# Performance work log

Measured on AMD Instinct MI355X. Metric: run time of the kernel, lower is better.

Reference implementation:

```python
import jax, jax.numpy as jnp
import numpy as np
from jax import lax

DIM = 512
HEADS = 8
SR = 2  # kernel_and_stride for the KV downsampling conv


def setup_inputs() -> dict:
    key = jax.random.key(0)
    k0, k1, k2, k3 = jax.random.split(key, 4)
    B, C, H, W = 4, DIM, 64, 64
    x = jax.random.normal(k0, (B, C, H, W), dtype=jnp.float32)
    # Conv weights in OIHW layout (matching torch)
    wq = jax.random.normal(k1, (C, C, 1, 1), dtype=jnp.float32) / np.sqrt(C)
    wkv = jax.random.normal(k2, (2 * C, C, SR, SR), dtype=jnp.float32) / np.sqrt(C * SR * SR)
    wout = jax.random.normal(k3, (C, C, 1, 1), dtype=jnp.float32) / np.sqrt(C)
    return {"x": x, "wq": wq, "wkv": wkv, "wout": wout}


def _attend(x, wq, wkv, wout):
    B, C, H, W = x.shape
    d = C // HEADS
    scale = d ** -0.5
    # to_q: 1x1 conv == channel matmul
    q = jnp.einsum('bchw,oc->bohw', x, wq[:, :, 0, 0])
    # to_kv: strided conv, downsamples spatial grid by SR
    kv = lax.conv_general_dilated(
        x, wkv, window_strides=(SR, SR), padding='VALID',
        dimension_numbers=('NCHW', 'OIHW', 'NCHW'))
    k, v = jnp.split(kv, 2, axis=1)  # each [B, C, H/SR, W/SR]

    def to_bhl(t):  # [B, (h d), X, Y] -> [B, h, X*Y, d]
        b, c, xh, xw = t.shape
        return t.reshape(b, HEADS, d, xh * xw).transpose(0, 1, 3, 2)

    qh, kh, vh = to_bhl(q), to_bhl(k), to_bhl(v)
    sim = jnp.einsum('bhid,bhjd->bhij', qh, kh) * scale
    attn = jax.nn.softmax(sim, axis=-1)
    out = jnp.einsum('bhij,bhjd->bhid', attn, vh)  # [B, h, HW, d]
    out = out.transpose(0, 1, 3, 2).reshape(B, C, H, W)
    return jnp.einsum('bchw,oc->bohw', out, wout[:, :, 0, 0])


def reference(x, wq, wkv, wout):
    return _attend(x, wq, wkv, wout)
```

## Files before the change

kernel.cpp:

```cpp
#include <hip/hip_runtime.h>
#include <hip/hip_bf16.h>

typedef __bf16 bf16x8 __attribute__((ext_vector_type(8)));
typedef float f32x4 __attribute__((ext_vector_type(4)));
typedef unsigned short ushort_t;
typedef ushort_t ushort8 __attribute__((ext_vector_type(8)));
typedef unsigned uint2v __attribute__((ext_vector_type(2)));
typedef unsigned uint4v __attribute__((ext_vector_type(4)));

#define DIM 512
#define HEADS 8
#define HD 64
#define HWN 4096
#define KVN 1024
#define KKV 2048
#define LOG2E 1.44269504f

__device__ __forceinline__ ushort_t f2bf(float f) {
    union { float f; unsigned u; } v; v.f = f;
    unsigned r = v.u + 0x7fffu + ((v.u >> 16) & 1u);
    return (ushort_t)(r >> 16);
}

__device__ __forceinline__ unsigned cvtpk(float lo, float hi) {
    unsigned r;
    asm("v_cvt_pk_bf16_f32 %0, %1, %2" : "=v"(r) : "v"(lo), "v"(hi));
    return r;
}

__device__ __forceinline__ void pl32swap(unsigned &a, unsigned &b) {
    asm("v_permlane32_swap_b32 %0, %1" : "+v"(a), "+v"(b));
}
__device__ __forceinline__ void pl16swap(unsigned &a, unsigned &b) {
    asm("v_permlane16_swap_b32 %0, %1" : "+v"(a), "+v"(b));
}

__device__ __forceinline__ bf16x8 frag4(unsigned a, unsigned b, unsigned c, unsigned d) {
    uint4v t; t[0] = a; t[1] = b; t[2] = c; t[3] = d;
    return __builtin_bit_cast(bf16x8, t);
}

__device__ __forceinline__ void gload_lds16(const ushort_t* g, ushort_t* l) {
    __builtin_amdgcn_global_load_lds(
        (const __attribute__((address_space(1))) unsigned int*)(const void*)g,
        (__attribute__((address_space(3))) unsigned int*)(void*)l,
        16, 0, 0);
}

__global__ __launch_bounds__(256) void cvt_kernel(
        const float* __restrict__ src, ushort_t* __restrict__ dst, int n8) {
    int i = blockIdx.x * 256 + threadIdx.x;
    if (i >= n8) return;
    const float* p = &src[(size_t)i * 8];
    f32x4 v0 = *(const f32x4*)&p[0];
    f32x4 v1 = *(const f32x4*)&p[4];
    ushort8 w;
    w[0] = f2bf(v0[0]); w[1] = f2bf(v0[1]); w[2] = f2bf(v0[2]); w[3] = f2bf(v0[3]);
    w[4] = f2bf(v1[0]); w[5] = f2bf(v1[1]); w[6] = f2bf(v1[2]); w[7] = f2bf(v1[3]);
    *(ushort8*)&dst[i * 8] = w;
}

__global__ __launch_bounds__(256) void cvt_xT_kernel(
        const float* __restrict__ x, ushort_t* __restrict__ xT) {
    const int b  = blockIdx.z;
    const int c0 = blockIdx.y * 64;
    const int p0 = blockIdx.x * 64;
    __shared__ ushort_t tile[64 * 72];

    const int tid = threadIdx.x;
    {
        int r = tid >> 2, pc = (tid & 3) * 16;
        const float* src = &x[((size_t)b * DIM + c0 + r) * HWN + p0 + pc];
        f32x4 v0 = *(const f32x4*)&src[0];
        f32x4 v1 = *(const f32x4*)&src[4];
        f32x4 v2 = *(const f32x4*)&src[8];
        f32x4 v3 = *(const f32x4*)&src[12];
        ushort8 w0, w1;
        w0[0]=f2bf(v0[0]); w0[1]=f2bf(v0[1]); w0[2]=f2bf(v0[2]); w0[3]=f2bf(v0[3]);
        w0[4]=f2bf(v1[0]); w0[5]=f2bf(v1[1]); w0[6]=f2bf(v1[2]); w0[7]=f2bf(v1[3]);
        w1[0]=f2bf(v2[0]); w1[1]=f2bf(v2[1]); w1[2]=f2bf(v2[2]); w1[3]=f2bf(v2[3]);
        w1[4]=f2bf(v3[0]); w1[5]=f2bf(v3[1]); w1[6]=f2bf(v3[2]); w1[7]=f2bf(v3[3]);
        *(ushort8*)&tile[r * 72 + pc]     = w0;
        *(ushort8*)&tile[r * 72 + pc + 8] = w1;
    }
    __syncthreads();
    {
        int p = tid >> 2, cc = (tid & 3) * 16;
        ushort8 w0, w1;
        #pragma unroll
        for (int j = 0; j < 8; ++j) {
            w0[j] = tile[(cc + j) * 72 + p];
            w1[j] = tile[(cc + 8 + j) * 72 + p];
        }
        ushort_t* dst = &xT[((size_t)b * HWN + p0 + p) * DIM + c0 + cc];
        *(ushort8*)&dst[0] = w0;
        *(ushort8*)&dst[8] = w1;
    }
}

__global__ __launch_bounds__(256) void cvt_wkvT_kernel(
        const float* __restrict__ wkv, ushort_t* __restrict__ wkvT) {
    int i = blockIdx.x * 256 + threadIdx.x;
    if (i >= 1024 * 512) return;
    int o2 = i >> 9, c = i & 511;
    f32x4 v = *(const f32x4*)&wkv[(size_t)i * 4];
    #pragma unroll
    for (int q = 0; q < 4; ++q)
        wkvT[(size_t)o2 * KKV + q * 512 + c] = f2bf(v[q]);
}

__global__ __launch_bounds__(256) void qproj_kernel(
        const ushort_t* __restrict__ xT, const ushort_t* __restrict__ wqb,
        ushort_t* __restrict__ qs) {
    const int b  = blockIdx.z;
    const int m0 = blockIdx.y * 64;
    const int p0 = blockIdx.x * 64;

    __shared__ ushort_t ldsA[64 * 40];
    __shared__ ushort_t ldsB[64 * 40];

    const int tid  = threadIdx.x;
    const int wave = tid >> 6;
    const int lane = tid & 63;
    const int l15  = lane & 15;
    const int quad = lane >> 4;
    const int mw   = (wave >> 1) * 32;
    const int nw   = (wave & 1) * 32;

    f32x4 zero = {0.f, 0.f, 0.f, 0.f};
    f32x4 acc[2][2] = {{zero, zero}, {zero, zero}};

    for (int k0 = 0; k0 < DIM; k0 += 32) {
        int row = tid >> 2, ko = (tid & 3) * 8;
        *(ushort8*)&ldsA[row * 40 + ko] =
            *(const ushort8*)&wqb[(m0 + row) * DIM + k0 + ko];
        *(ushort8*)&ldsB[row * 40 + ko] =
            *(const ushort8*)&xT[((size_t)b * HWN + p0 + row) * DIM + k0 + ko];
        __syncthreads();
        bf16x8 a0 = *(const bf16x8*)&ldsA[(mw + l15) * 40 + quad * 8];
        bf16x8 a1 = *(const bf16x8*)&ldsA[(mw + 16 + l15) * 40 + quad * 8];
        bf16x8 b0 = *(const bf16x8*)&ldsB[(nw + l15) * 40 + quad * 8];
        bf16x8 b1 = *(const bf16x8*)&ldsB[(nw + 16 + l15) * 40 + quad * 8];
        acc[0][0] = __builtin_amdgcn_mfma_f32_16x16x32_bf16(a0, b0, acc[0][0], 0, 0, 0);
        acc[0][1] = __builtin_amdgcn_mfma_f32_16x16x32_bf16(a0, b1, acc[0][1], 0, 0, 0);
        acc[1][0] = __builtin_amdgcn_mfma_f32_16x16x32_bf16(a1, b0, acc[1][0], 0, 0, 0);
        acc[1][1] = __builtin_amdgcn_mfma_f32_16x16x32_bf16(a1, b1, acc[1][1], 0, 0, 0);
        __syncthreads();
    }

    #pragma unroll
    for (int mi = 0; mi < 2; ++mi)
        #pragma unroll
        for (int ni = 0; ni < 2; ++ni)
            #pragma unroll
            for (int r = 0; r < 4; ++r) {
                int m = m0 + mw + mi * 16 + quad * 4 + r;
                int n = p0 + nw + ni * 16 + l15;
                qs[((size_t)b * DIM + m) * HWN + n] =
                    f2bf(acc[mi][ni][r] * (0.125f * LOG2E));
            }
}

__global__ __launch_bounds__(256) void kv_kernel(
        const ushort_t* __restrict__ xT, const ushort_t* __restrict__ wkvT,
        ushort_t* __restrict__ ks, ushort_t* __restrict__ vt) {
    const int b  = blockIdx.z;
    const int m0 = blockIdx.y * 64;
    const int j0 = blockIdx.x * 64;

    __shared__ ushort_t ldsA[64 * 40];
    __shared__ ushort_t ldsB[64 * 40];
    __shared__ ushort_t cbuf[64 * 72];

    const int tid  = threadIdx.x;
    const int wave = tid >> 6;
    const int lane = tid & 63;
    const int l15  = lane & 15;
    const int quad = lane >> 4;
    const int mw   = (wave >> 1) * 32;
    const int nw   = (wave & 1) * 32;

    f32x4 zero = {0.f, 0.f, 0.f, 0.f};
    f32x4 acc[2][2] = {{zero, zero}, {zero, zero}};

    const int row = tid >> 2, ko = (tid & 3) * 8;
    const int yj = (j0 + row) >> 5, xj = (j0 + row) & 31;

    for (int k0 = 0; k0 < KKV; k0 += 32) {
        int q  = k0 >> 9;
        int c0 = k0 & 511;
        int di = q >> 1, dj = q & 1;
        int p  = (2 * yj + di) * 64 + 2 * xj + dj;
        *(ushort8*)&ldsA[row * 40 + ko] =
            *(const ushort8*)&wkvT[(size_t)(m0 + row) * KKV + k0 + ko];
        *(ushort8*)&ldsB[row * 40 + ko] =
            *(const ushort8*)&xT[((size_t)b * HWN + p) * DIM + c0 + ko];
        __syncthreads();
        bf16x8 a0 = *(const bf16x8*)&ldsA[(mw + l15) * 40 + quad * 8];
        bf16x8 a1 = *(const bf16x8*)&ldsA[(mw + 16 + l15) * 40 + quad * 8];
        bf16x8 b0 = *(const bf16x8*)&ldsB[(nw + l15) * 40 + quad * 8];
        bf16x8 b1 = *(const bf16x8*)&ldsB[(nw + 16 + l15) * 40 + quad * 8];
        acc[0][0] = __builtin_amdgcn_mfma_f32_16x16x32_bf16(a0, b0, acc[0][0], 0, 0, 0);
        acc[0][1] = __builtin_amdgcn_mfma_f32_16x16x32_bf16(a0, b1, acc[0][1], 0, 0, 0);
        acc[1][0] = __builtin_amdgcn_mfma_f32_16x16x32_bf16(a1, b0, acc[1][0], 0, 0, 0);
        acc[1][1] = __builtin_amdgcn_mfma_f32_16x16x32_bf16(a1, b1, acc[1][1], 0, 0, 0);
        __syncthreads();
    }

    if (m0 < DIM) {
        int h = m0 >> 6;
        #pragma unroll
        for (int mi = 0; mi < 2; ++mi)
            #pragma unroll
            for (int ni = 0; ni < 2; ++ni)
                #pragma unroll
                for (int r = 0; r < 4; ++r) {
                    int m = mw + mi * 16 + quad * 4 + r;
                    int n = nw + ni * 16 + l15;
                    cbuf[n * 72 + m] = f2bf(acc[mi][ni][r]);
                }
        __syncthreads();
        int n = tid >> 2, mo = (tid & 3) * 16;
        ushort8 v0 = *(const ushort8*)&cbuf[n * 72 + mo];
        ushort8 v1 = *(const ushort8*)&cbuf[n * 72 + mo + 8];
        ushort_t* dst = &ks[(((size_t)b * HEADS + h) * KVN + j0 + n) * HD + mo];
        *(ushort8*)&dst[0] = v0;
        *(ushort8*)&dst[8] = v1;
    } else {
        int h = (m0 - DIM) >> 6;
        #pragma unroll
        for (int mi = 0; mi < 2; ++mi)
            #pragma unroll
            for (int ni = 0; ni < 2; ++ni)
                #pragma unroll
                for (int r = 0; r < 4; ++r) {
                    int dd = mw + mi * 16 + quad * 4 + r;
                    int n  = nw + ni * 16 + l15;
                    vt[(((size_t)b * HEADS + h) * HD + dd) * KVN + j0 + n] =
                        f2bf(acc[mi][ni][r]);
                }
    }
}

__global__ __launch_bounds__(256, 2) void attn_kernel(
        const ushort_t* __restrict__ qs,
        const ushort_t* __restrict__ ks,
        const ushort_t* __restrict__ vt,
        ushort_t* __restrict__ ao) {
    const int b = blockIdx.z, h = blockIdx.y;
    const int tid = threadIdx.x, wave = tid >> 6, lane = tid & 63;
    const int l15 = lane & 15, quad = lane >> 4;
    const int s7  = l15 & 7;
    const int iw = blockIdx.x * 256 + wave * 64;

    __shared__ ushort_t ldsK[2][64 * 64];
    __shared__ ushort_t ldsV[2][64 * 64];

    const ushort_t* Kh = &ks[((size_t)b * HEADS + h) * (KVN * HD)];
    const ushort_t* Vh = &vt[((size_t)b * HEADS + h) * (HD * KVN)];

    const int srow = wave * 8 + (lane >> 3);
    const int schk = (lane & 7) ^ (lane >> 3);
    const ushort_t* kp0 = Kh + srow * HD + schk * 8;
    const ushort_t* kp1 = Kh + (srow + 32) * HD + schk * 8;
    const ushort_t* vp0 = Vh + (size_t)srow * KVN + schk * 8;
    const ushort_t* vp1 = Vh + (size_t)(srow + 32) * KVN + schk * 8;

    bf16x8 bq[4][2];
    #pragma unroll
    for (int ih = 0; ih < 4; ++ih)
        #pragma unroll
        for (int kk = 0; kk < 2; ++kk) {
            ushort8 t;
            #pragma unroll
            for (int j = 0; j < 8; ++j) {
                int c = h * HD + kk * 32 + quad * 8 + j;
                int p = iw + ih * 16 + l15;
                t[j] = qs[((size_t)b * DIM + c) * HWN + p];
            }
            bq[ih][kk] = *(bf16x8*)&t;
        }

    f32x4 zero = {0.f, 0.f, 0.f, 0.f};
    f32x4 o[4][4];
    #pragma unroll
    for (int ih = 0; ih < 4; ++ih)
        #pragma unroll
        for (int nt = 0; nt < 4; ++nt) o[ih][nt] = zero;
    float ssum[4] = {0.f, 0.f, 0.f, 0.f};

    gload_lds16(kp0, &ldsK[0][wave * 512]);
    gload_lds16(kp1, &ldsK[0][wave * 512 + 2048]);
    gload_lds16(vp0, &ldsV[0][wave * 512]);
    gload_lds16(vp1, &ldsV[0][wave * 512 + 2048]);
    asm volatile("s_waitcnt vmcnt(0)" ::: "memory");
    __syncthreads();

    for (int t = 0; t < 16; ++t) {
        const int cur = t & 1;
        if (t < 15) {
            const int jn = (t + 1) * 64;
            gload_lds16(kp0 + jn * HD, &ldsK[cur ^ 1][wave * 512]);
            gload_lds16(kp1 + jn * HD, &ldsK[cur ^ 1][wave * 512 + 2048]);
            gload_lds16(vp0 + jn,      &ldsV[cur ^ 1][wave * 512]);
            gload_lds16(vp1 + jn,      &ldsV[cur ^ 1][wave * 512 + 2048]);
        }

        unsigned P2[4][4][2];
        #pragma unroll
        for (int nt = 0; nt < 4; ++nt) {
            const ushort_t* kb = &ldsK[cur][(nt * 16 + l15) * 64];
            bf16x8 bk0 = *(const bf16x8*)&kb[(quad ^ s7) * 8];
            bf16x8 bk1 = *(const bf16x8*)&kb[((quad + 4) ^ s7) * 8];
            #pragma unroll
            for (int ih = 0; ih < 4; ++ih) {
                f32x4 s = zero;
                s = __builtin_amdgcn_mfma_f32_16x16x32_bf16(bk0, bq[ih][0], s, 0, 0, 0);
                s = __builtin_amdgcn_mfma_f32_16x16x32_bf16(bk1, bq[ih][1], s, 0, 0, 0);
                float p0 = __builtin_amdgcn_exp2f(s[0]);
                float p1 = __builtin_amdgcn_exp2f(s[1]);
                float p2 = __builtin_amdgcn_exp2f(s[2]);
                float p3 = __builtin_amdgcn_exp2f(s[3]);
                ssum[ih] += (p0 + p1) + (p2 + p3);
                P2[ih][nt][0] = cvtpk(p0, p1);
                P2[ih][nt][1] = cvtpk(p2, p3);
            }
        }

        #pragma unroll
        for (int ih = 0; ih < 4; ++ih)
            #pragma unroll
            for (int bh = 0; bh < 2; ++bh)
                #pragma unroll
                for (int rp = 0; rp < 2; ++rp) {
                    pl32swap(P2[ih][bh * 2][rp], P2[ih][bh * 2 + 1][rp]);
                    pl16swap(P2[ih][bh * 2][rp], P2[ih][bh * 2 + 1][rp]);
                }
        bf16x8 bp[4][2];
        #pragma unroll
        for (int ih = 0; ih < 4; ++ih) {
            bp[ih][0] = frag4(P2[ih][0][0], P2[ih][0][1], P2[ih][1][0], P2[ih][1][1]);
            bp[ih][1] = frag4(P2[ih][2][0], P2[ih][2][1], P2[ih][3][0], P2[ih][3][1]);
        }

        #pragma unroll
        for (int nt = 0; nt < 4; ++nt) {
            const ushort_t* vb = &ldsV[cur][(nt * 16 + l15) * 64];
            bf16x8 bv0 = *(const bf16x8*)&vb[(quad ^ s7) * 8];
            bf16x8 bv1 = *(const bf16x8*)&vb[((quad + 4) ^ s7) * 8];
            #pragma unroll
            for (int ih = 0; ih < 4; ++ih) {
                o[ih][nt] = __builtin_amdgcn_mfma_f32_16x16x32_bf16(bv0, bp[ih][0], o[ih][nt], 0, 0, 0);
                o[ih][nt] = __builtin_amdgcn_mfma_f32_16x16x32_bf16(bv1, bp[ih][1], o[ih][nt], 0, 0, 0);
            }
        }

        asm volatile("s_waitcnt vmcnt(0)" ::: "memory");
        __syncthreads();
    }

    #pragma unroll
    for (int ih = 0; ih < 4; ++ih) {
        float tsum = ssum[ih];
        tsum += __shfl_xor(tsum, 16);
        tsum += __shfl_xor(tsum, 32);
        float invl = 1.0f / tsum;
        int i = iw + ih * 16 + l15;
        ushort_t* dst = &ao[((size_t)b * HWN + i) * DIM + h * HD];
        #pragma unroll
        for (int nt = 0; nt < 4; ++nt) {
            unsigned d0 = cvtpk(o[ih][nt][0] * invl, o[ih][nt][1] * invl);
            unsigned d1 = cvtpk(o[ih][nt][2] * invl, o[ih][nt][3] * invl);
            uint2v w; w[0] = d0; w[1] = d1;
            *(uint2v*)&dst[nt * 16 + quad * 4] = w;
        }
    }
}

__global__ __launch_bounds__(256) void outproj_kernel(
        const ushort_t* __restrict__ ao, const ushort_t* __restrict__ woutb,
        float* __restrict__ out) {
    const int b  = blockIdx.z;
    const int m0 = blockIdx.y * 64;
    const int p0 = blockIdx.x * 64;

    __shared__ ushort_t ldsA[64 * 40];
    __shared__ ushort_t ldsB[64 * 40];

    const int tid  = threadIdx.x;
    const int wave = tid >> 6;
    const int lane = tid & 63;
    const int l15  = lane & 15;
    const int quad = lane >> 4;
    const int mw   = (wave >> 1) * 32;
    const int nw   = (wave & 1) * 32;

    f32x4 zero = {0.f, 0.f, 0.f, 0.f};
    f32x4 acc[2][2] = {{zero, zero}, {zero, zero}};

    for (int k0 = 0; k0 < DIM; k0 += 32) {
        int row = tid >> 2, ko = (tid & 3) * 8;
        *(ushort8*)&ldsA[row * 40 + ko] =
            *(const ushort8*)&woutb[(m0 + row) * DIM + k0 + ko];
        *(ushort8*)&ldsB[row * 40 + ko] =
            *(const ushort8*)&ao[((size_t)b * HWN + p0 + row) * DIM + k0 + ko];
        __syncthreads();
        bf16x8 a0 = *(const bf16x8*)&ldsA[(mw + l15) * 40 + quad * 8];
        bf16x8 a1 = *(const bf16x8*)&ldsA[(mw + 16 + l15) * 40 + quad * 8];
        bf16x8 b0 = *(const bf16x8*)&ldsB[(nw + l15) * 40 + quad * 8];
        bf16x8 b1 = *(const bf16x8*)&ldsB[(nw + 16 + l15) * 40 + quad * 8];
        acc[0][0] = __builtin_amdgcn_mfma_f32_16x16x32_bf16(a0, b0, acc[0][0], 0, 0, 0);
        acc[0][1] = __builtin_amdgcn_mfma_f32_16x16x32_bf16(a0, b1, acc[0][1], 0, 0, 0);
        acc[1][0] = __builtin_amdgcn_mfma_f32_16x16x32_bf16(a1, b0, acc[1][0], 0, 0, 0);
        acc[1][1] = __builtin_amdgcn_mfma_f32_16x16x32_bf16(a1, b1, acc[1][1], 0, 0, 0);
        __syncthreads();
    }

    #pragma unroll
    for (int mi = 0; mi < 2; ++mi)
        #pragma unroll
        for (int ni = 0; ni < 2; ++ni)
            #pragma unroll
            for (int r = 0; r < 4; ++r) {
                int m = m0 + mw + mi * 16 + quad * 4 + r;
                int n = p0 + nw + ni * 16 + l15;
                out[((size_t)b * DIM + m) * HWN + n] = acc[mi][ni][r];
            }
}

extern "C" void kernel_launch(void* const* d_in, const int* in_sizes, int n_in,
                              void* d_out, int out_size, void* d_ws, size_t ws_size,
                              hipStream_t stream) {
    const float* x    = (const float*)d_in[0];
    const float* wq   = (const float*)d_in[1];
    const float* wkv  = (const float*)d_in[2];
    const float* wout = (const float*)d_in[3];
    float* out = (float*)d_out;

    char* ws = (char*)d_ws;
    ushort_t* xT    = (ushort_t*)(ws);
    ushort_t* qsb   = (ushort_t*)(ws + 16777216);
    ushort_t* ksb   = (ushort_t*)(ws + 33554432);
    ushort_t* vtb   = (ushort_t*)(ws + 37748736);
    ushort_t* aob   = (ushort_t*)(ws + 41943040);
    ushort_t* wqb   = (ushort_t*)(ws + 58720256);
    ushort_t* wkvT  = (ushort_t*)(ws + 59244544);
    ushort_t* woutb = (ushort_t*)(ws + 63438848);

    cvt_xT_kernel  <<<dim3(64, 8, 4), 256, 0, stream>>>(x, xT);
    cvt_kernel     <<<dim3(128),      256, 0, stream>>>(wq, wqb, 32768);
    cvt_wkvT_kernel<<<dim3(2048),     256, 0, stream>>>(wkv, wkvT);
    cvt_kernel     <<<dim3(128),      256, 0, stream>>>(wout, woutb, 32768);

    qproj_kernel  <<<dim3(64, 8, 4),  256, 0, stream>>>(xT, wqb, qsb);
    kv_kernel     <<<dim3(16, 16, 4), 256, 0, stream>>>(xT, wkvT, ksb, vtb);
    attn_kernel   <<<dim3(16, 8, 4),  256, 0, stream>>>(qsb, ksb, vtb, aob);
    outproj_kernel<<<dim3(64, 8, 4),  256, 0, stream>>>(aob, woutb, out);
}
```

Before: 231.2 us.

## Enlarge projection GEMM tiles to 128x128 and stage operands via direct global-to-LDS loads

The q-projection, kv-projection and output-projection GEMMs move from 64x64 to 128x128 block tiles, with each wave computing a 64x64 sub-tile from a 4x4 grid of MFMA fragments. Operand tiles now go straight from global memory into LDS with global_load_lds, replacing the register round-trip, and the padded LDS stride is dropped. The aim is more MFMA work per LDS read and per global byte, plus fewer blocks and less redundant operand traffic. In exchange each thread holds four times the accumulator registers, there are fewer blocks to fill the GPU, and the unpadded stride-32 LDS layout may cause bank conflicts. The K-output epilogue is also reworked to transpose two head slices through shared memory in turn.

```diff
diff --git a/kernel.cpp b/kernel.cpp
--- a/kernel.cpp
+++ b/kernel.cpp
@@ -45,6 +45,23 @@
         (const __attribute__((address_space(1))) unsigned int*)(const void*)g,
         (__attribute__((address_space(3))) unsigned int*)(void*)l,
         16, 0, 0);
+}
+
+__device__ __forceinline__ void kstep_mfma(
+        const ushort_t* __restrict__ ldsA, const ushort_t* __restrict__ ldsB,
+        int wm, int wn, int l15, int quad, f32x4 (&acc)[4][4]) {
+    bf16x8 a[4], bb[4];
+    #pragma unroll
+    for (int i = 0; i < 4; ++i)
+        a[i] = *(const bf16x8*)&ldsA[(wm + i * 16 + l15) * 32 + quad * 8];
+    #pragma unroll
+    for (int j = 0; j < 4; ++j)
+        bb[j] = *(const bf16x8*)&ldsB[(wn + j * 16 + l15) * 32 + quad * 8];
+    #pragma unroll
+    for (int i = 0; i < 4; ++i)
+        #pragma unroll
+        for (int j = 0; j < 4; ++j)
+            acc[i][j] = __builtin_amdgcn_mfma_f32_16x16x32_bf16(a[i], bb[j], acc[i][j], 0, 0, 0);
 }
 
 __global__ __launch_bounds__(256) void cvt_kernel(
@@ -113,51 +130,54 @@
         const ushort_t* __restrict__ xT, const ushort_t* __restrict__ wqb,
         ushort_t* __restrict__ qs) {
     const int b  = blockIdx.z;
-    const int m0 = blockIdx.y * 64;
-    const int p0 = blockIdx.x * 64;
-
-    __shared__ ushort_t ldsA[64 * 40];
-    __shared__ ushort_t ldsB[64 * 40];
+    const int m0 = blockIdx.y * 128;
+    const int n0 = blockIdx.x * 128;
+
+    __shared__ ushort_t ldsA[128 * 32];
+    __shared__ ushort_t ldsB[128 * 32];
 
     const int tid  = threadIdx.x;
     const int wave = tid >> 6;
     const int lane = tid & 63;
     const int l15  = lane & 15;
     const int quad = lane >> 4;
-    const int mw   = (wave >> 1) * 32;
-    const int nw   = (wave & 1) * 32;
+    const int wm   = (wave >> 1) * 64;
+    const int wn   = (wave & 1) * 64;
+
+    const int srow = wave * 32 + (lane >> 2);
+    const int schk = (lane & 3) * 8;
+    const ushort_t* asrc = &wqb[(m0 + srow) * DIM + schk];
+    const ushort_t* bsrc = &xT[((size_t)b * HWN + n0 + srow) * DIM + schk];
+    ushort_t* adst = &ldsA[wave * 1024];
+    ushort_t* bdst = &ldsB[wave * 1024];
 
     f32x4 zero = {0.f, 0.f, 0.f, 0.f};
-    f32x4 acc[2][2] = {{zero, zero}, {zero, zero}};
+    f32x4 acc[4][4];
+    #pragma unroll
+    for (int i = 0; i < 4; ++i)
+        #pragma unroll
+        for (int j = 0; j < 4; ++j) acc[i][j] = zero;
 
     for (int k0 = 0; k0 < DIM; k0 += 32) {
-        int row = tid >> 2, ko = (tid & 3) * 8;
-        *(ushort8*)&ldsA[row * 40 + ko] =
-            *(const ushort8*)&wqb[(m0 + row) * DIM + k0 + ko];
-        *(ushort8*)&ldsB[row * 40 + ko] =
-            *(const ushort8*)&xT[((size_t)b * HWN + p0 + row) * DIM + k0 + ko];
+        gload_lds16(asrc + k0,            adst);
+        gload_lds16(asrc + 16 * DIM + k0, adst + 512);
+        gload_lds16(bsrc + k0,            bdst);
+        gload_lds16(bsrc + 16 * DIM + k0, bdst + 512);
         __syncthreads();
-        bf16x8 a0 = *(const bf16x8*)&ldsA[(mw + l15) * 40 + quad * 8];
-        bf16x8 a1 = *(const bf16x8*)&ldsA[(mw + 16 + l15) * 40 + quad * 8];
-        bf16x8 b0 = *(const bf16x8*)&ldsB[(nw + l15) * 40 + quad * 8];
-        bf16x8 b1 = *(const bf16x8*)&ldsB[(nw + 16 + l15) * 40 + quad * 8];
-        acc[0][0] = __builtin_amdgcn_mfma_f32_16x16x32_bf16(a0, b0, acc[0][0], 0, 0, 0);
-        acc[0][1] = __builtin_amdgcn_mfma_f32_16x16x32_bf16(a0, b1, acc[0][1], 0, 0, 0);
-        acc[1][0] = __builtin_amdgcn_mfma_f32_16x16x32_bf16(a1, b0, acc[1][0], 0, 0, 0);
-        acc[1][1] = __builtin_amdgcn_mfma_f32_16x16x32_bf16(a1, b1, acc[1][1], 0, 0, 0);
+        kstep_mfma(ldsA, ldsB, wm, wn, l15, quad, acc);
         __syncthreads();
     }
 
     #pragma unroll
-    for (int mi = 0; mi < 2; ++mi)
-        #pragma unroll
-        for (int ni = 0; ni < 2; ++ni)
+    for (int i = 0; i < 4; ++i)
+        #pragma unroll
+        for (int j = 0; j < 4; ++j)
             #pragma unroll
             for (int r = 0; r < 4; ++r) {
-                int m = m0 + mw + mi * 16 + quad * 4 + r;
-                int n = p0 + nw + ni * 16 + l15;
+                int m = m0 + wm + i * 16 + quad * 4 + r;
+                int n = n0 + wn + j * 16 + l15;
                 qs[((size_t)b * DIM + m) * HWN + n] =
-                    f2bf(acc[mi][ni][r] * (0.125f * LOG2E));
+                    f2bf(acc[i][j][r] * (0.125f * LOG2E));
             }
 }
 
@@ -165,79 +185,100 @@
         const ushort_t* __restrict__ xT, const ushort_t* __restrict__ wkvT,
         ushort_t* __restrict__ ks, ushort_t* __restrict__ vt) {
     const int b  = blockIdx.z;
-    const int m0 = blockIdx.y * 64;
-    const int j0 = blockIdx.x * 64;
-
-    __shared__ ushort_t ldsA[64 * 40];
-    __shared__ ushort_t ldsB[64 * 40];
-    __shared__ ushort_t cbuf[64 * 72];
+    const int m0 = blockIdx.y * 128;
+    const int j0 = blockIdx.x * 128;
+
+    __shared__ ushort_t sh[128 * 72];
+    ushort_t* ldsA = sh;
+    ushort_t* ldsB = sh + 4096;
 
     const int tid  = threadIdx.x;
     const int wave = tid >> 6;
     const int lane = tid & 63;
     const int l15  = lane & 15;
     const int quad = lane >> 4;
-    const int mw   = (wave >> 1) * 32;
-    const int nw   = (wave & 1) * 32;
+    const int wm   = (wave >> 1) * 64;
+    const int wn   = (wave & 1) * 64;
+
+    const int srow = wave * 32 + (lane >> 2);
+    const int schk = (lane & 3) * 8;
+    const int jr0 = j0 + srow, jr1 = jr0 + 16;
+    const int y0 = jr0 >> 5, x0 = jr0 & 31;
+    const int y1 = jr1 >> 5, x1 = jr1 & 31;
+
+    const ushort_t* asrc = &wkvT[(size_t)(m0 + srow) * KKV + schk];
+    ushort_t* adst = &ldsA[wave * 1024];
+    ushort_t* bdst = &ldsB[wave * 1024];
 
     f32x4 zero = {0.f, 0.f, 0.f, 0.f};
-    f32x4 acc[2][2] = {{zero, zero}, {zero, zero}};
-
-    const int row = tid >> 2, ko = (tid & 3) * 8;
-    const int yj = (j0 + row) >> 5, xj = (j0 + row) & 31;
-
-    for (int k0 = 0; k0 < KKV; k0 += 32) {
-        int q  = k0 >> 9;
-        int c0 = k0 & 511;
-        int di = q >> 1, dj = q & 1;
-        int p  = (2 * yj + di) * 64 + 2 * xj + dj;
-        *(ushort8*)&ldsA[row * 40 + ko] =
-            *(const ushort8*)&wkvT[(size_t)(m0 + row) * KKV + k0 + ko];
-        *(ushort8*)&ldsB[row * 40 + ko] =
-            *(const ushort8*)&xT[((size_t)b * HWN + p) * DIM + c0 + ko];
-        __syncthreads();
-        bf16x8 a0 = *(const bf16x8*)&ldsA[(mw + l15) * 40 + quad * 8];
-        bf16x8 a1 = *(const bf16x8*)&ldsA[(mw + 16 + l15) * 40 + quad * 8];
-        bf16x8 b0 = *(const bf16x8*)&ldsB[(nw + l15) * 40 + quad * 8];
-        bf16x8 b1 = *(const bf16x8*)&ldsB[(nw + 16 + l15) * 40 + quad * 8];
-        acc[0][0] = __builtin_amdgcn_mfma_f32_16x16x32_bf16(a0, b0, acc[0][0], 0, 0, 0);
-        acc[0][1] = __builtin_amdgcn_mfma_f32_16x16x32_bf16(a0, b1, acc[0][1], 0, 0, 0);
-        acc[1][0] = __builtin_amdgcn_mfma_f32_16x16x32_bf16(a1, b0, acc[1][0], 0, 0, 0);
-        acc[1][1] = __builtin_amdgcn_mfma_f32_16x16x32_bf16(a1, b1, acc[1][1], 0, 0, 0);
-        __syncthreads();
+    f32x4 acc[4][4];
+    #pragma unroll
+    for (int i = 0; i < 4; ++i)
+        #pragma unroll
+        for (int j = 0; j < 4; ++j) acc[i][j] = zero;
+
+    for (int q = 0; q < 4; ++q) {
+        const int di = q >> 1, dj = q & 1;
+        const ushort_t* b0 =
+            &xT[((size_t)b * HWN + (2 * y0 + di) * 64 + 2 * x0 + dj) * DIM + schk];
+        const ushort_t* b1 =
+            &xT[((size_t)b * HWN + (2 * y1 + di) * 64 + 2 * x1 + dj) * DIM + schk];
+        const ushort_t* aq = asrc + q * 512;
+        for (int kc = 0; kc < 512; kc += 32) {
+            gload_lds16(aq + kc,                    adst);
+            gload_lds16(aq + 16 * KKV + kc,         adst + 512);
+            gload_lds16(b0 + kc,                    bdst);
+            gload_lds16(b1 + kc,                    bdst + 512);
+            __syncthreads();
+            kstep_mfma(ldsA, ldsB, wm, wn, l15, quad, acc);
+            __syncthreads();
+        }
     }
 
     if (m0 < DIM) {
-        int h = m0 >> 6;
-        #pragma unroll
-        for (int mi = 0; mi < 2; ++mi)
-            #pragma unroll
-            for (int ni = 0; ni < 2; ++ni)
+        const int h0 = m0 >> 6;
+        #pragma unroll
+        for (int mh = 0; mh < 2; ++mh) {
+            if ((wave >> 1) == mh) {
+                #pragma unroll
+                for (int i = 0; i < 4; ++i)
+                    #pragma unroll
+                    for (int j = 0; j < 4; ++j)
+                        #pragma unroll
+                        for (int r = 0; r < 4; ++r) {
+                            int mloc = i * 16 + quad * 4 + r;
+                            int n    = wn + j * 16 + l15;
+                            sh[n * 72 + mloc] = f2bf(acc[i][j][r]);
+                        }
+            }
+            __syncthreads();
+            {
+                int n = tid >> 1, doff = (tid & 1) * 32;
+                ushort8 u0 = *(const ushort8*)&sh[n * 72 + doff];
+                ushort8 u1 = *(const ushort8*)&sh[n * 72 + doff + 8];
+                ushort8 u2 = *(const ushort8*)&sh[n * 72 + doff + 16];
+                ushort8 u3 = *(const ushort8*)&sh[n * 72 + doff + 24];
+                ushort_t* dst =
+                    &ks[(((size_t)b * HEADS + h0 + mh) * KVN + j0 + n) * HD + doff];
+                *(ushort8*)&dst[0]  = u0;
+                *(ushort8*)&dst[8]  = u1;
+                *(ushort8*)&dst[16] = u2;
+                *(ushort8*)&dst[24] = u3;
+            }
+            __syncthreads();
+        }
+    } else {
+        #pragma unroll
+        for (int i = 0; i < 4; ++i)
+            #pragma unroll
+            for (int j = 0; j < 4; ++j)
                 #pragma unroll
                 for (int r = 0; r < 4; ++r) {
-                    int m = mw + mi * 16 + quad * 4 + r;
-                    int n = nw + ni * 16 + l15;
-                    cbuf[n * 72 + m] = f2bf(acc[mi][ni][r]);
-                }
-        __syncthreads();
-        int n = tid >> 2, mo = (tid & 3) * 16;
-        ushort8 v0 = *(const ushort8*)&cbuf[n * 72 + mo];
-        ushort8 v1 = *(const ushort8*)&cbuf[n * 72 + mo + 8];
-        ushort_t* dst = &ks[(((size_t)b * HEADS + h) * KVN + j0 + n) * HD + mo];
-        *(ushort8*)&dst[0] = v0;
-        *(ushort8*)&dst[8] = v1;
-    } else {
-        int h = (m0 - DIM) >> 6;
-        #pragma unroll
-        for (int mi = 0; mi < 2; ++mi)
-            #pragma unroll
-            for (int ni = 0; ni < 2; ++ni)
-                #pragma unroll
-                for (int r = 0; r < 4; ++r) {
-                    int dd = mw + mi * 16 + quad * 4 + r;
-                    int n  = nw + ni * 16 + l15;
+                    int mfull = m0 - DIM + wm + i * 16 + quad * 4 + r;
+                    int h  = mfull >> 6, dd = mfull & 63;
+                    int n  = wn + j * 16 + l15;
                     vt[(((size_t)b * HEADS + h) * HD + dd) * KVN + j0 + n] =
-                        f2bf(acc[mi][ni][r]);
+                        f2bf(acc[i][j][r]);
                 }
     }
 }
@@ -381,50 +422,53 @@
         const ushort_t* __restrict__ ao, const ushort_t* __restrict__ woutb,
         float* __restrict__ out) {
     const int b  = blockIdx.z;
-    const int m0 = blockIdx.y * 64;
-    const int p0 = blockIdx.x * 64;
-
-    __shared__ ushort_t ldsA[64 * 40];
-    __shared__ ushort_t ldsB[64 * 40];
+    const int m0 = blockIdx.y * 128;
+    const int n0 = blockIdx.x * 128;
+
+    __shared__ ushort_t ldsA[128 * 32];
+    __shared__ ushort_t ldsB[128 * 32];
 
     const int tid  = threadIdx.x;
     const int wave = tid >> 6;
     const int lane = tid & 63;
     const int l15  = lane & 15;
     const int quad = lane >> 4;
-    const int mw   = (wave >> 1) * 32;
-    const int nw   = (wave & 1) * 32;
+    const int wm   = (wave >> 1) * 64;
+    const int wn   = (wave & 1) * 64;
+
+    const int srow = wave * 32 + (lane >> 2);
+    const int schk = (lane & 3) * 8;
+    const ushort_t* asrc = &woutb[(m0 + srow) * DIM + schk];
+    const ushort_t* bsrc = &ao[((size_t)b * HWN + n0 + srow) * DIM + schk];
+    ushort_t* adst = &ldsA[wave * 1024];
+    ushort_t* bdst = &ldsB[wave * 1024];
 
     f32x4 zero = {0.f, 0.f, 0.f, 0.f};
-    f32x4 acc[2][2] = {{zero, zero}, {zero, zero}};
+    f32x4 acc[4][4];
+    #pragma unroll
+    for (int i = 0; i < 4; ++i)
+        #pragma unroll
+        for (int j = 0; j < 4; ++j) acc[i][j] = zero;
 
     for (int k0 = 0; k0 < DIM; k0 += 32) {
-        int row = tid >> 2, ko = (tid & 3) * 8;
-        *(ushort8*)&ldsA[row * 40 + ko] =
-            *(const ushort8*)&woutb[(m0 + row) * DIM + k0 + ko];
-        *(ushort8*)&ldsB[row * 40 + ko] =
-            *(const ushort8*)&ao[((size_t)b * HWN + p0 + row) * DIM + k0 + ko];
+        gload_lds16(asrc + k0,            adst);
+        gload_lds16(asrc + 16 * DIM + k0, adst + 512);
+        gload_lds16(bsrc + k0,            bdst);
+        gload_lds16(bsrc + 16 * DIM + k0, bdst + 512);
         __syncthreads();
-        bf16x8 a0 = *(const bf16x8*)&ldsA[(mw + l15) * 40 + quad * 8];
-        bf16x8 a1 = *(const bf16x8*)&ldsA[(mw + 16 + l15) * 40 + quad * 8];
-        bf16x8 b0 = *(const bf16x8*)&ldsB[(nw + l15) * 40 + quad * 8];
-        bf16x8 b1 = *(const bf16x8*)&ldsB[(nw + 16 + l15) * 40 + quad * 8];
-        acc[0][0] = __builtin_amdgcn_mfma_f32_16x16x32_bf16(a0, b0, acc[0][0], 0, 0, 0);
-        acc[0][1] = __builtin_amdgcn_mfma_f32_16x16x32_bf16(a0, b1, acc[0][1], 0, 0, 0);
-        acc[1][0] = __builtin_amdgcn_mfma_f32_16x16x32_bf16(a1, b0, acc[1][0], 0, 0, 0);
-        acc[1][1] = __builtin_amdgcn_mfma_f32_16x16x32_bf16(a1, b1, acc[1][1], 0, 0, 0);
+        kstep_mfma(ldsA, ldsB, wm, wn, l15, quad, acc);
         __syncthreads();
     }
 
     #pragma unroll
-    for (int mi = 0; mi < 2; ++mi)
-        #pragma unroll
-        for (int ni = 0; ni < 2; ++ni)
+    for (int i = 0; i < 4; ++i)
+        #pragma unroll
+        for (int j = 0; j < 4; ++j)
             #pragma unroll
             for (int r = 0; r < 4; ++r) {
-                int m = m0 + mw + mi * 16 + quad * 4 + r;
-                int n = p0 + nw + ni * 16 + l15;
-                out[((size_t)b * DIM + m) * HWN + n] = acc[mi][ni][r];
+                int m = m0 + wm + i * 16 + quad * 4 + r;
+                int n = n0 + wn + j * 16 + l15;
+                out[((size_t)b * DIM + m) * HWN + n] = acc[i][j][r];
             }
 }
 
@@ -452,8 +496,8 @@
     cvt_wkvT_kernel<<<dim3(2048),     256, 0, stream>>>(wkv, wkvT);
     cvt_kernel     <<<dim3(128),      256, 0, stream>>>(wout, woutb, 32768);
 
-    qproj_kernel  <<<dim3(64, 8, 4),  256, 0, stream>>>(xT, wqb, qsb);
-    kv_kernel     <<<dim3(16, 16, 4), 256, 0, stream>>>(xT, wkvT, ksb, vtb);
+    qproj_kernel  <<<dim3(32, 4, 4),  256, 0, stream>>>(xT, wqb, qsb);
+    kv_kernel     <<<dim3(8, 8, 4),   256, 0, stream>>>(xT, wkvT, ksb, vtb);
     attn_kernel   <<<dim3(16, 8, 4),  256, 0, stream>>>(qsb, ksb, vtb, aob);
-    outproj_kernel<<<dim3(64, 8, 4),  256, 0, stream>>>(aob, woutb, out);
-}
+    outproj_kernel<<<dim3(32, 4, 4),  256, 0, stream>>>(aob, woutb, out);
+}
```

Measured after the change: 218.0 us. -5.7%, faster.
